# Optimization experiments

Hardware: AMD Instinct MI355X
Metric: run time of the kernel (lower is better)

Reference implementation:

```python
import jax, jax.numpy as jnp
import numpy as np

NP, P, H, NB = 14, 16, 12, 6  # n_patches per side, patch size, heads, blocks
HD, EMB, SEQ = 64, 768, NP * NP + 1


def _layernorm(x, g, b, eps=1e-5):
    m = x.mean(axis=-1, keepdims=True)
    v = x.var(axis=-1, keepdims=True)
    return (x - m) * jax.lax.rsqrt(v + eps) * g + b


def setup_inputs() -> dict:
    key = jax.random.key(0)
    ks = jax.random.split(key, 16)
    s = 0.02
    B = 64
    inp = {
        "images": jax.random.normal(ks[0], (B, 3, 224, 224), jnp.float32),
        "Wmap": jax.random.normal(ks[1], (768, 768), jnp.float32) * s,
        "bmap": jnp.zeros((768,), jnp.float32),
        "cls_tok": jax.random.normal(ks[2], (1, 768), jnp.float32) * s,
        "pos": jax.random.normal(ks[3], (SEQ, 768), jnp.float32) * s,
        "ln1_g": jnp.ones((NB, 768), jnp.float32),
        "ln1_b": jnp.zeros((NB, 768), jnp.float32),
        "Wq": jax.random.normal(ks[4], (NB, H, HD, HD), jnp.float32) * s,
        "bq": jnp.zeros((NB, H, HD), jnp.float32),
        "Wk": jax.random.normal(ks[5], (NB, H, HD, HD), jnp.float32) * s,
        "bk": jnp.zeros((NB, H, HD), jnp.float32),
        "Wv": jax.random.normal(ks[6], (NB, H, HD, HD), jnp.float32) * s,
        "bv": jnp.zeros((NB, H, HD), jnp.float32),
        "ln2_g": jnp.ones((NB, 768), jnp.float32),
        "ln2_b": jnp.zeros((NB, 768), jnp.float32),
        "W1": jax.random.normal(ks[7], (NB, 768, 3072), jnp.float32) * s,
        "b1": jnp.zeros((NB, 3072), jnp.float32),
        "W2": jax.random.normal(ks[8], (NB, 3072, 768), jnp.float32) * s,
        "b2": jnp.zeros((NB, 768), jnp.float32),
        "Whead": jax.random.normal(ks[9], (768, 10), jnp.float32) * s,
        "bhead": jnp.zeros((10,), jnp.float32),
    }
    return inp


def reference(images, Wmap, bmap, cls_tok, pos, ln1_g, ln1_b, Wq, bq, Wk, bk,
              Wv, bv, ln2_g, ln2_b, W1, b1, W2, b2, Whead, bhead):
    B = images.shape[0]
    # patchify: (B,3,224,224) -> (B,196,768); per-patch channel-first flatten
    x = images.reshape(B, 3, NP, P, NP, P)
    x = x.transpose(0, 2, 4, 1, 3, 5).reshape(B, NP * NP, 3 * P * P)
    tokens = x @ Wmap + bmap  # (B,196,768)
    tokens = jnp.concatenate(
        [jnp.broadcast_to(cls_tok[None], (B, 1, EMB)), tokens], axis=1)
    out = tokens + pos[None]  # (B,197,768)
    scale = 1.0 / jnp.sqrt(jnp.asarray(H, out.dtype))  # NOTE: source divides by sqrt(num_heads)
    for i in range(NB):
        h = _layernorm(out, ln1_g[i], ln1_b[i])
        xh = h.reshape(B, SEQ, H, HD)
        q = jnp.einsum('bshd,hde->bshe', xh, Wq[i]) + bq[i]
        k = jnp.einsum('bshd,hde->bshe', xh, Wk[i]) + bk[i]
        v = jnp.einsum('bshd,hde->bshe', xh, Wv[i]) + bv[i]
        attn = jax.nn.softmax(
            jnp.einsum('bqhd,bkhd->bhqk', q, k) * scale, axis=-1)
        o = jnp.einsum('bhqk,bkhd->bqhd', attn, v).reshape(B, SEQ, EMB)
        out = out + o
        h2 = _layernorm(out, ln2_g[i], ln2_b[i])
        mlp = jax.nn.gelu(h2 @ W1[i] + b1[i], approximate=False) @ W2[i] + b2[i]
        out = out + mlp
    cls = out[:, 0]  # (B,768)
    return jax.nn.softmax(cls @ Whead + bhead, axis=-1)
```

## Files before the change

### kernel.cpp

```cpp
#include <hip/hip_runtime.h>
#include <cstddef>

#define BATCH 64
#define SEQL  197
#define EMB   768
#define NH    12
#define HDIM  64
#define NBLK  6
#define MLPD  3072
#define TOKS  12608
#define PTOK  12544
#define ATT_SCALE 0.28867513459481287f
#define LOG2E 1.4426950408889634f

typedef short bf16x8 __attribute__((ext_vector_type(8)));
typedef float f32x4  __attribute__((ext_vector_type(4)));

__device__ inline float bf2f(unsigned short u) {
  union { unsigned int i; float f; } c; c.i = ((unsigned int)u) << 16; return c.f;
}
__device__ inline unsigned short f2bf(float f) {
  union { float f; unsigned int i; } c; c.f = f;
  unsigned int r = c.i + 0x7FFFu + ((c.i >> 16) & 1u);
  return (unsigned short)(r >> 16);
}

__device__ __forceinline__ float gelu_f(float x) {
  float u = __builtin_fabsf(x) * 0.70710678118654752f;
  float t = __builtin_amdgcn_rcpf(__builtin_fmaf(0.3275911f, u, 1.0f));
  float p = __builtin_fmaf(1.061405429f, t, -1.453152027f);
  p = __builtin_fmaf(p, t, 1.421413741f);
  p = __builtin_fmaf(p, t, -0.284496736f);
  p = __builtin_fmaf(p, t, 0.254829592f);
  p = p * t;
  float e = __expf(-u * u);
  float er = __builtin_fmaf(-p, e, 1.0f);
  er = __builtin_copysignf(er, x);
  return 0.5f * x * (1.0f + er);
}

__device__ __forceinline__ void gload16(const unsigned short* g, void* l) {
  __builtin_amdgcn_global_load_lds(
      (const __attribute__((address_space(1))) unsigned int*)g,
      (__attribute__((address_space(3))) unsigned int*)l, 16, 0, 0);
}

__global__ __launch_bounds__(256) void patchify_kernel(const float* __restrict__ img,
                                                       unsigned short* __restrict__ out) {
  int i4 = blockIdx.x * 256 + threadIdx.x;
  int f4 = i4 % 192;
  int r  = i4 / 192;
  int b  = r / 196, t = r - b * 196;
  int f  = f4 * 4;
  int c  = f >> 8;
  int rem = f & 255;
  int iy = rem >> 4, ix = rem & 15;
  int py = t / 14, px = t - py * 14;
  const float* src = img + ((((size_t)b * 3 + c) * 224 + py * 16 + iy) * 224 + px * 16 + ix);
  float4 v = *(const float4*)src;
  ushort4 u;
  u.x = f2bf(v.x); u.y = f2bf(v.y); u.z = f2bf(v.z); u.w = f2bf(v.w);
  *(ushort4*)(out + (size_t)r * 768 + f) = u;
}

__global__ __launch_bounds__(256) void clspos_kernel(const float* __restrict__ cls,
                                                     const float* __restrict__ pos,
                                                     float* __restrict__ X) {
  int idx = blockIdx.x * 256 + threadIdx.x;
  int b = idx / 768, e = idx - b * 768;
  X[(size_t)b * SEQL * 768 + e] = cls[e] + pos[e];
}

__global__ __launch_bounds__(256) void wconv_kernel(const float* __restrict__ W,
                                                    unsigned short* __restrict__ Wt,
                                                    int K, int N) {
  __shared__ float t[32][33];
  int k0 = blockIdx.x * 32, n0 = blockIdx.y * 32;
  int kk = threadIdx.x >> 3, nn = (threadIdx.x & 7) * 4;
  float4 v = *(const float4*)&W[(size_t)(k0 + kk) * N + n0 + nn];
  t[nn + 0][kk] = v.x; t[nn + 1][kk] = v.y; t[nn + 2][kk] = v.z; t[nn + 3][kk] = v.w;
  __syncthreads();
  int nr = threadIdx.x >> 3, kc = (threadIdx.x & 7) * 4;
  ushort4 u;
  u.x = f2bf(t[nr][kc + 0]); u.y = f2bf(t[nr][kc + 1]);
  u.z = f2bf(t[nr][kc + 2]); u.w = f2bf(t[nr][kc + 3]);
  *(ushort4*)&Wt[(size_t)(n0 + nr) * K + k0 + kc] = u;
}

__global__ __launch_bounds__(256) void qwconv_kernel(const float* __restrict__ Wq,
                                                     const float* __restrict__ Wk,
                                                     const float* __restrict__ Wv,
                                                     unsigned short* __restrict__ Wt) {
  int mh = blockIdx.x;
  int m = mh / 12, h = mh - m * 12;
  const float* src = (m == 0 ? Wq : (m == 1 ? Wk : Wv)) + (size_t)h * 4096;
  unsigned short* dst = Wt + (size_t)mh * 4096;
  for (int idx = threadIdx.x; idx < 4096; idx += 256) {
    int d = idx >> 6, e = idx & 63;
    dst[e * 64 + d] = f2bf(src[idx]);
  }
}

template<int MODE>
__global__ __launch_bounds__(256) void gemm_mfma(const unsigned short* __restrict__ A, int lda,
                                                 const unsigned short* __restrict__ Bt, int ldb,
                                                 void* __restrict__ Cv,
                                                 const float* __restrict__ bias,
                                                 const float* __restrict__ pos,
                                                 int M, int N, int K) {
  __shared__ short As[8192];
  __shared__ short Bs[8192];
  const int tid  = threadIdx.x;
  const int wid  = tid >> 6, lane = tid & 63;
  const int wr   = wid >> 1, wc = wid & 1;
  const int fr   = lane & 15;
  const int fq   = lane >> 4;
  const int m0   = blockIdx.y * 128;
  const int n0   = blockIdx.x * 128;
  const int srow = lane >> 3;
  const int schk = lane & 7;
  const int Mc   = M - 1;

  f32x4 acc[4][4];
#pragma unroll
  for (int m = 0; m < 4; ++m)
#pragma unroll
    for (int n = 0; n < 4; ++n) acc[m][n] = (f32x4)0.f;

  for (int k0 = 0; k0 < K; k0 += 64) {
#pragma unroll
    for (int i = 0; i < 4; ++i) {
      int row = i * 32 + wid * 8 + srow;
      int gr = m0 + row; if (gr > Mc) gr = Mc;
      gload16(A + (size_t)gr * lda + k0 + ((schk ^ (row & 7)) << 3),
              (char*)As + i * 4096 + wid * 1024);
      gload16(Bt + (size_t)(n0 + row) * ldb + k0 + ((schk ^ (row & 7)) << 3),
              (char*)Bs + i * 4096 + wid * 1024);
    }
    __syncthreads();
#pragma unroll
    for (int ks = 0; ks < 2; ++ks) {
      bf16x8 af[4], bfr[4];
#pragma unroll
      for (int m = 0; m < 4; ++m) {
        int row = (wr << 6) + (m << 4) + fr;
        int ch = ((ks << 2) + fq) ^ (row & 7);
        af[m] = *(const bf16x8*)&As[(row << 6) + (ch << 3)];
      }
#pragma unroll
      for (int n = 0; n < 4; ++n) {
        int row = (wc << 6) + (n << 4) + fr;
        int ch = ((ks << 2) + fq) ^ (row & 7);
        bfr[n] = *(const bf16x8*)&Bs[(row << 6) + (ch << 3)];
      }
#pragma unroll
      for (int m = 0; m < 4; ++m)
#pragma unroll
        for (int n = 0; n < 4; ++n)
          acc[m][n] = __builtin_amdgcn_mfma_f32_16x16x32_bf16(af[m], bfr[n], acc[m][n], 0, 0, 0);
    }
    __syncthreads();
  }

#pragma unroll
  for (int m = 0; m < 4; ++m) {
#pragma unroll
    for (int j = 0; j < 4; ++j) {
      int r = m0 + (wr << 6) + (m << 4) + (fq << 2) + j;
      if (r >= M) continue;
#pragma unroll
      for (int n = 0; n < 4; ++n) {
        int c = n0 + (wc << 6) + (n << 4) + fr;
        float v = acc[m][n][j] + bias[c];
        if (MODE == 0) {
          int b = r / 196, t = r - b * 196;
          ((float*)Cv)[((size_t)b * SEQL + 1 + t) * 768 + c] = v + pos[(size_t)(1 + t) * 768 + c];
        } else if (MODE == 1) {
          ((unsigned short*)Cv)[(size_t)r * MLPD + c] = f2bf(gelu_f(v));
        } else {
          ((float*)Cv)[(size_t)r * 768 + c] += v;
        }
      }
    }
  }
}

__global__ __launch_bounds__(256) void ln_kernel(const float* __restrict__ Xi,
                                                 unsigned short* __restrict__ Ho,
                                                 const float* __restrict__ g,
                                                 const float* __restrict__ bb) {
  int tok = blockIdx.x * 4 + (threadIdx.x >> 6);
  int lane = threadIdx.x & 63;
  const float* x = Xi + (size_t)tok * 768;
  float4 v0 = *(const float4*)(x + lane * 4);
  float4 v1 = *(const float4*)(x + 256 + lane * 4);
  float4 v2 = *(const float4*)(x + 512 + lane * 4);
  float s = v0.x + v0.y + v0.z + v0.w + v1.x + v1.y + v1.z + v1.w + v2.x + v2.y + v2.z + v2.w;
  float q = v0.x*v0.x + v0.y*v0.y + v0.z*v0.z + v0.w*v0.w
          + v1.x*v1.x + v1.y*v1.y + v1.z*v1.z + v1.w*v1.w
          + v2.x*v2.x + v2.y*v2.y + v2.z*v2.z + v2.w*v2.w;
#pragma unroll
  for (int o = 32; o > 0; o >>= 1) { s += __shfl_xor(s, o); q += __shfl_xor(q, o); }
  float mean = s * (1.f / 768.f);
  float var  = q * (1.f / 768.f) - mean * mean;
  float rs = rsqrtf(var + 1e-5f);
  unsigned short* outp = Ho + (size_t)tok * 768;
  float4 g0 = *(const float4*)(g + lane * 4);
  float4 g1 = *(const float4*)(g + 256 + lane * 4);
  float4 g2 = *(const float4*)(g + 512 + lane * 4);
  float4 b0 = *(const float4*)(bb + lane * 4);
  float4 b1 = *(const float4*)(bb + 256 + lane * 4);
  float4 b2 = *(const float4*)(bb + 512 + lane * 4);
  ushort4 s0, s1, s2;
  s0.x = f2bf((v0.x - mean) * rs * g0.x + b0.x); s0.y = f2bf((v0.y - mean) * rs * g0.y + b0.y);
  s0.z = f2bf((v0.z - mean) * rs * g0.z + b0.z); s0.w = f2bf((v0.w - mean) * rs * g0.w + b0.w);
  s1.x = f2bf((v1.x - mean) * rs * g1.x + b1.x); s1.y = f2bf((v1.y - mean) * rs * g1.y + b1.y);
  s1.z = f2bf((v1.z - mean) * rs * g1.z + b1.z); s1.w = f2bf((v1.w - mean) * rs * g1.w + b1.w);
  s2.x = f2bf((v2.x - mean) * rs * g2.x + b2.x); s2.y = f2bf((v2.y - mean) * rs * g2.y + b2.y);
  s2.z = f2bf((v2.z - mean) * rs * g2.z + b2.z); s2.w = f2bf((v2.w - mean) * rs * g2.w + b2.w);
  *(ushort4*)(outp + lane * 4) = s0;
  *(ushort4*)(outp + 256 + lane * 4) = s1;
  *(ushort4*)(outp + 512 + lane * 4) = s2;
}

__global__ __launch_bounds__(256) void qkv_mfma(const unsigned short* __restrict__ Hb,
    const unsigned short* __restrict__ Wt,
    const float* __restrict__ bq, const float* __restrict__ bk, const float* __restrict__ bv,
    unsigned short* __restrict__ Qo, unsigned short* __restrict__ Ko,
    unsigned short* __restrict__ Vo) {
  const int h = blockIdx.y;
  const int tid = threadIdx.x, wv = tid >> 6, lane = tid & 63;
  const int fr = lane & 15, hi = lane >> 4;
  const int t0 = blockIdx.x * 64 + wv * 16;
  const unsigned short* arow = Hb + (size_t)(t0 + fr) * 768 + h * 64;
  bf16x8 a0 = *(const bf16x8*)(arow + hi * 8);
  bf16x8 a1 = *(const bf16x8*)(arow + 32 + hi * 8);
  f32x4 acc[3][4];
#pragma unroll
  for (int m = 0; m < 3; ++m)
#pragma unroll
    for (int n = 0; n < 4; ++n) acc[m][n] = (f32x4)0.f;
#pragma unroll
  for (int m = 0; m < 3; ++m) {
    const unsigned short* wb = Wt + (size_t)(m * 12 + h) * 4096;
#pragma unroll
    for (int n = 0; n < 4; ++n) {
      bf16x8 b0 = *(const bf16x8*)&wb[(n * 16 + fr) * 64 + hi * 8];
      bf16x8 b1 = *(const bf16x8*)&wb[(n * 16 + fr) * 64 + 32 + hi * 8];
      acc[m][n] = __builtin_amdgcn_mfma_f32_16x16x32_bf16(a0, b0, acc[m][n], 0, 0, 0);
      acc[m][n] = __builtin_amdgcn_mfma_f32_16x16x32_bf16(a1, b1, acc[m][n], 0, 0, 0);
    }
  }
#pragma unroll
  for (int m = 0; m < 3; ++m) {
    const float* bptr = (m == 0 ? bq : (m == 1 ? bk : bv)) + h * 64;
    unsigned short* optr = (m == 0 ? Qo : (m == 1 ? Ko : Vo));
    const float sc = (m == 0) ? ATT_SCALE : 1.f;
#pragma unroll
    for (int j = 0; j < 4; ++j) {
      int tk = t0 + hi * 4 + j;
      int b = tk / 197, s = tk - b * 197;
      size_t base_o = (((size_t)b * NH + h) * SEQL + s) * 64;
#pragma unroll
      for (int n = 0; n < 4; ++n)
        optr[base_o + n * 16 + fr] = f2bf((acc[m][n][j] + bptr[n * 16 + fr]) * sc);
    }
  }
}

__global__ __launch_bounds__(256) void attn_kernel(const unsigned short* __restrict__ Q,
                                                   const unsigned short* __restrict__ Kg,
                                                   const unsigned short* __restrict__ Vg,
                                                   float* __restrict__ X) {
  __shared__ unsigned short Vt[64][232];
  __shared__ unsigned short Pl[4][16][232];
  const int bh = blockIdx.x;
  const int b = bh / NH, h = bh - b * NH;
  const int tid = threadIdx.x, wv = tid >> 6, lane = tid & 63;
  const int fr = lane & 15, hi = lane >> 4;
  const unsigned short* Qp = Q  + (size_t)bh * SEQL * 64;
  const unsigned short* Kp = Kg + (size_t)bh * SEQL * 64;
  const unsigned short* Vp = Vg + (size_t)bh * SEQL * 64;

  for (int idx = tid; idx < SEQL * 16; idx += 256) {
    int s = idx >> 4, d4 = (idx & 15) * 4;
    ushort4 v = *(const ushort4*)&Vp[s * 64 + d4];
    Vt[d4 + 0][s] = v.x; Vt[d4 + 1][s] = v.y; Vt[d4 + 2][s] = v.z; Vt[d4 + 3][s] = v.w;
  }
  for (int idx = tid; idx < 64 * 35; idx += 256) {
    int d = idx / 35, c = 197 + idx % 35;
    Vt[d][c] = 0;
  }
  for (int idx = lane; idx < 16 * 24; idx += 64) {
    int r = idx / 24, c = 208 + idx % 24;
    Pl[wv][r][c] = 0;
  }
  __syncthreads();

  for (int qt = wv; qt < 13; qt += 4) {
    int qrow = qt * 16 + fr; if (qrow > 196) qrow = 196;
    bf16x8 qa0 = *(const bf16x8*)&Qp[qrow * 64 + hi * 8];
    bf16x8 qa1 = *(const bf16x8*)&Qp[qrow * 64 + 32 + hi * 8];
    f32x4 sc[13];
#pragma unroll
    for (int kt = 0; kt < 13; ++kt) {
      int krow = kt * 16 + fr; if (krow > 196) krow = 196;
      bf16x8 kb0 = *(const bf16x8*)&Kp[krow * 64 + hi * 8];
      bf16x8 kb1 = *(const bf16x8*)&Kp[krow * 64 + 32 + hi * 8];
      f32x4 a = (f32x4)0.f;
      a = __builtin_amdgcn_mfma_f32_16x16x32_bf16(qa0, kb0, a, 0, 0, 0);
      a = __builtin_amdgcn_mfma_f32_16x16x32_bf16(qa1, kb1, a, 0, 0, 0);
      sc[kt] = a;
    }
    float mx[4] = {-3e38f, -3e38f, -3e38f, -3e38f};
#pragma unroll
    for (int kt = 0; kt < 13; ++kt) {
      bool inval = (kt == 12) && (fr >= 5);
#pragma unroll
      for (int j = 0; j < 4; ++j) {
        float s = inval ? -3e38f : sc[kt][j];
        sc[kt][j] = s;
        mx[j] = fmaxf(mx[j], s);
      }
    }
#pragma unroll
    for (int o = 8; o > 0; o >>= 1)
#pragma unroll
      for (int j = 0; j < 4; ++j) mx[j] = fmaxf(mx[j], __shfl_xor(mx[j], o));
    float l[4] = {0.f, 0.f, 0.f, 0.f};
#pragma unroll
    for (int kt = 0; kt < 13; ++kt) {
#pragma unroll
      for (int j = 0; j < 4; ++j) {
        float p = exp2f((sc[kt][j] - mx[j]) * LOG2E);
        if ((kt == 12) && (fr >= 5)) p = 0.f;
        l[j] += p;
        Pl[wv][hi * 4 + j][kt * 16 + fr] = f2bf(p);
      }
    }
#pragma unroll
    for (int o = 8; o > 0; o >>= 1)
#pragma unroll
      for (int j = 0; j < 4; ++j) l[j] += __shfl_xor(l[j], o);
    f32x4 ov[4];
#pragma unroll
    for (int n = 0; n < 4; ++n) ov[n] = (f32x4)0.f;
#pragma unroll
    for (int kc = 0; kc < 7; ++kc) {
      bf16x8 pa = *(const bf16x8*)&Pl[wv][fr][kc * 32 + hi * 8];
#pragma unroll
      for (int n = 0; n < 4; ++n) {
        bf16x8 vb = *(const bf16x8*)&Vt[n * 16 + fr][kc * 32 + hi * 8];
        ov[n] = __builtin_amdgcn_mfma_f32_16x16x32_bf16(pa, vb, ov[n], 0, 0, 0);
      }
    }
#pragma unroll
    for (int j = 0; j < 4; ++j) {
      int r = qt * 16 + hi * 4 + j;
      if (r >= SEQL) continue;
      float inv = 1.f / l[j];
      float* xp = X + ((size_t)b * SEQL + r) * 768 + h * 64 + fr;
#pragma unroll
      for (int n = 0; n < 4; ++n) xp[n * 16] += ov[n][j] * inv;
    }
  }
}

__global__ __launch_bounds__(64) void head_kernel(const float* __restrict__ X,
                                                  const float* __restrict__ Wh,
                                                  const float* __restrict__ bh,
                                                  float* __restrict__ out) {
  __shared__ float lg[10];
  int b = blockIdx.x, t = threadIdx.x;
  if (t < 10) {
    float acc = bh[t];
    const float* x = X + (size_t)b * SEQL * 768;
    for (int d = 0; d < 768; ++d) acc += x[d] * Wh[d * 10 + t];
    lg[t] = acc;
  }
  __syncthreads();
  if (t == 0) {
    float m = lg[0];
    for (int c = 1; c < 10; ++c) m = fmaxf(m, lg[c]);
    float ssum = 0.f;
    for (int c = 0; c < 10; ++c) ssum += expf(lg[c] - m);
    for (int c = 0; c < 10; ++c) out[b * 10 + c] = expf(lg[c] - m) / ssum;
  }
}

extern "C" void kernel_launch(void* const* d_in, const int* in_sizes, int n_in,
                              void* d_out, int out_size, void* d_ws, size_t ws_size,
                              hipStream_t stream) {
  const float* images = (const float*)d_in[0];
  const float* Wmap = (const float*)d_in[1];
  const float* bmap = (const float*)d_in[2];
  const float* cls  = (const float*)d_in[3];
  const float* pos  = (const float*)d_in[4];
  const float* ln1g = (const float*)d_in[5];
  const float* ln1b = (const float*)d_in[6];
  const float* Wq   = (const float*)d_in[7];
  const float* bq   = (const float*)d_in[8];
  const float* Wk   = (const float*)d_in[9];
  const float* bk   = (const float*)d_in[10];
  const float* Wv   = (const float*)d_in[11];
  const float* bv   = (const float*)d_in[12];
  const float* ln2g = (const float*)d_in[13];
  const float* ln2b = (const float*)d_in[14];
  const float* W1   = (const float*)d_in[15];
  const float* b1   = (const float*)d_in[16];
  const float* W2   = (const float*)d_in[17];
  const float* b2   = (const float*)d_in[18];
  const float* Wh   = (const float*)d_in[19];
  const float* bhd  = (const float*)d_in[20];
  float* out = (float*)d_out;

  const size_t ACT = (size_t)TOKS * 768;
  const size_t oX = 0;
  const size_t oHb = oX + ACT * 4;
  const size_t oR  = oHb + ACT * 2;
  const size_t oW1 = oR + 3 * ACT * 4;
  const size_t oW2 = oW1 + (size_t)768 * 3072 * 2;
  const size_t oWm = oW2 + (size_t)768 * 3072 * 2;
  const size_t oQW = oWm + (size_t)768 * 768 * 2;
  const size_t need = oQW + (size_t)36 * 4096 * 2;
  if (ws_size < need) return;

  char* ws = (char*)d_ws;
  float* X = (float*)(ws + oX);
  unsigned short* Hb = (unsigned short*)(ws + oHb);
  unsigned short* Qb = (unsigned short*)(ws + oR);
  unsigned short* Kb = Qb + ACT;
  unsigned short* Vb = Kb + ACT;
  unsigned short* mid = (unsigned short*)(ws + oR);
  unsigned short* patches = (unsigned short*)(ws + oR);
  unsigned short* W1t = (unsigned short*)(ws + oW1);
  unsigned short* W2t = (unsigned short*)(ws + oW2);
  unsigned short* Wmapt = (unsigned short*)(ws + oWm);
  unsigned short* QWt = (unsigned short*)(ws + oQW);

  wconv_kernel<<<dim3(24, 24), 256, 0, stream>>>(Wmap, Wmapt, 768, 768);
  patchify_kernel<<<9408, 256, 0, stream>>>(images, patches);
  clspos_kernel<<<192, 256, 0, stream>>>(cls, pos, X);
  gemm_mfma<0><<<dim3(6, 98), 256, 0, stream>>>(patches, 768, Wmapt, 768, X, bmap, pos,
                                                PTOK, 768, 768);

  for (int i = 0; i < NBLK; ++i) {
    ln_kernel<<<3152, 256, 0, stream>>>(X, Hb, ln1g + i * 768, ln1b + i * 768);
    qwconv_kernel<<<36, 256, 0, stream>>>(Wq + (size_t)i * 49152, Wk + (size_t)i * 49152,
                                          Wv + (size_t)i * 49152, QWt);
    qkv_mfma<<<dim3(197, 12), 256, 0, stream>>>(Hb, QWt,
        bq + i * 768, bk + i * 768, bv + i * 768, Qb, Kb, Vb);
    attn_kernel<<<768, 256, 0, stream>>>(Qb, Kb, Vb, X);
    ln_kernel<<<3152, 256, 0, stream>>>(X, Hb, ln2g + i * 768, ln2b + i * 768);
    wconv_kernel<<<dim3(24, 96), 256, 0, stream>>>(W1 + (size_t)i * 2359296, W1t, 768, MLPD);
    wconv_kernel<<<dim3(96, 24), 256, 0, stream>>>(W2 + (size_t)i * 2359296, W2t, MLPD, 768);
    gemm_mfma<1><<<dim3(24, 99), 256, 0, stream>>>(Hb, 768, W1t, 768, mid, b1 + i * MLPD,
                                                   nullptr, TOKS, MLPD, 768);
    gemm_mfma<2><<<dim3(6, 99), 256, 0, stream>>>(mid, MLPD, W2t, MLPD, X, b2 + i * 768,
                                                  nullptr, TOKS, 768, MLPD);
  }
  head_kernel<<<64, 64, 0, stream>>>(X, Wh, bhd, out);
}
```

Measured before the change: 1.920 ms.

## Vectorize GELU and Q/K epilogue stores via column-permuted layouts

The MLP1 epilogue now packs four bf16 outputs per lane into one ushort4 store. This places columns in a permuted order within each 64-column group of the intermediate activation, and W2 is converted with a matching K-permutation so the second GEMM still computes the right contraction. Q and K are stored the same way with a permuted head dimension, which cancels in the QK dot product, while V keeps the original layout. The aim is fewer, wider global stores, in exchange for a layout coupling across kernels that must stay consistent.

```diff
diff --git a/kernel.cpp b/kernel.cpp
--- a/kernel.cpp
+++ b/kernel.cpp
@@ -73,7 +73,7 @@
 
 __global__ __launch_bounds__(256) void wconv_kernel(const float* __restrict__ W,
                                                     unsigned short* __restrict__ Wt,
-                                                    int K, int N) {
+                                                    int K, int N, int perm) {
   __shared__ float t[32][33];
   int k0 = blockIdx.x * 32, n0 = blockIdx.y * 32;
   int kk = threadIdx.x >> 3, nn = (threadIdx.x & 7) * 4;
@@ -84,7 +84,17 @@
   ushort4 u;
   u.x = f2bf(t[nr][kc + 0]); u.y = f2bf(t[nr][kc + 1]);
   u.z = f2bf(t[nr][kc + 2]); u.w = f2bf(t[nr][kc + 3]);
-  *(ushort4*)&Wt[(size_t)(n0 + nr) * K + k0 + kc] = u;
+  if (!perm) {
+    *(ushort4*)&Wt[(size_t)(n0 + nr) * K + k0 + kc] = u;
+  } else {
+    size_t base = (size_t)(n0 + nr) * K + (size_t)(k0 & ~63);
+    int klo = (k0 & 32) + kc;
+    size_t st = base + (size_t)((klo & 15) * 4 + (klo >> 4));
+    Wt[st + 0]  = u.x;
+    Wt[st + 4]  = u.y;
+    Wt[st + 8]  = u.z;
+    Wt[st + 12] = u.w;
+  }
 }
 
 __global__ __launch_bounds__(256) void qwconv_kernel(const float* __restrict__ Wq,
@@ -168,17 +178,28 @@
     for (int j = 0; j < 4; ++j) {
       int r = m0 + (wr << 6) + (m << 4) + (fq << 2) + j;
       if (r >= M) continue;
-#pragma unroll
-      for (int n = 0; n < 4; ++n) {
-        int c = n0 + (wc << 6) + (n << 4) + fr;
-        float v = acc[m][n][j] + bias[c];
-        if (MODE == 0) {
-          int b = r / 196, t = r - b * 196;
-          ((float*)Cv)[((size_t)b * SEQL + 1 + t) * 768 + c] = v + pos[(size_t)(1 + t) * 768 + c];
-        } else if (MODE == 1) {
-          ((unsigned short*)Cv)[(size_t)r * MLPD + c] = f2bf(gelu_f(v));
-        } else {
-          ((float*)Cv)[(size_t)r * 768 + c] += v;
+      if (MODE == 1) {
+        ushort4 q;
+        float v0 = acc[0 * 0 + m][0][j] + bias[n0 + (wc << 6) + 0 * 16 + fr];
+        float v1 = acc[m][1][j] + bias[n0 + (wc << 6) + 1 * 16 + fr];
+        float v2 = acc[m][2][j] + bias[n0 + (wc << 6) + 2 * 16 + fr];
+        float v3 = acc[m][3][j] + bias[n0 + (wc << 6) + 3 * 16 + fr];
+        q.x = f2bf(gelu_f(v0));
+        q.y = f2bf(gelu_f(v1));
+        q.z = f2bf(gelu_f(v2));
+        q.w = f2bf(gelu_f(v3));
+        *(ushort4*)&((unsigned short*)Cv)[(size_t)r * MLPD + n0 + (wc << 6) + fr * 4] = q;
+      } else {
+#pragma unroll
+        for (int n = 0; n < 4; ++n) {
+          int c = n0 + (wc << 6) + (n << 4) + fr;
+          float v = acc[m][n][j] + bias[c];
+          if (MODE == 0) {
+            int b = r / 196, t = r - b * 196;
+            ((float*)Cv)[((size_t)b * SEQL + 1 + t) * 768 + c] = v + pos[(size_t)(1 + t) * 768 + c];
+          } else {
+            ((float*)Cv)[(size_t)r * 768 + c] += v;
+          }
         }
       }
     }
@@ -261,9 +282,18 @@
       int tk = t0 + hi * 4 + j;
       int b = tk / 197, s = tk - b * 197;
       size_t base_o = (((size_t)b * NH + h) * SEQL + s) * 64;
-#pragma unroll
-      for (int n = 0; n < 4; ++n)
-        optr[base_o + n * 16 + fr] = f2bf((acc[m][n][j] + bptr[n * 16 + fr]) * sc);
+      if (m < 2) {
+        ushort4 o;
+        o.x = f2bf((acc[m][0][j] + bptr[0 * 16 + fr]) * sc);
+        o.y = f2bf((acc[m][1][j] + bptr[1 * 16 + fr]) * sc);
+        o.z = f2bf((acc[m][2][j] + bptr[2 * 16 + fr]) * sc);
+        o.w = f2bf((acc[m][3][j] + bptr[3 * 16 + fr]) * sc);
+        *(ushort4*)&optr[base_o + fr * 4] = o;
+      } else {
+#pragma unroll
+        for (int n = 0; n < 4; ++n)
+          optr[base_o + n * 16 + fr] = f2bf(acc[m][n][j] + bptr[n * 16 + fr]);
+      }
     }
   }
 }
@@ -438,7 +468,7 @@
   unsigned short* Wmapt = (unsigned short*)(ws + oWm);
   unsigned short* QWt = (unsigned short*)(ws + oQW);
 
-  wconv_kernel<<<dim3(24, 24), 256, 0, stream>>>(Wmap, Wmapt, 768, 768);
+  wconv_kernel<<<dim3(24, 24), 256, 0, stream>>>(Wmap, Wmapt, 768, 768, 0);
   patchify_kernel<<<9408, 256, 0, stream>>>(images, patches);
   clspos_kernel<<<192, 256, 0, stream>>>(cls, pos, X);
   gemm_mfma<0><<<dim3(6, 98), 256, 0, stream>>>(patches, 768, Wmapt, 768, X, bmap, pos,
@@ -452,8 +482,8 @@
         bq + i * 768, bk + i * 768, bv + i * 768, Qb, Kb, Vb);
     attn_kernel<<<768, 256, 0, stream>>>(Qb, Kb, Vb, X);
     ln_kernel<<<3152, 256, 0, stream>>>(X, Hb, ln2g + i * 768, ln2b + i * 768);
-    wconv_kernel<<<dim3(24, 96), 256, 0, stream>>>(W1 + (size_t)i * 2359296, W1t, 768, MLPD);
-    wconv_kernel<<<dim3(96, 24), 256, 0, stream>>>(W2 + (size_t)i * 2359296, W2t, MLPD, 768);
+    wconv_kernel<<<dim3(24, 96), 256, 0, stream>>>(W1 + (size_t)i * 2359296, W1t, 768, MLPD, 0);
+    wconv_kernel<<<dim3(96, 24), 256, 0, stream>>>(W2 + (size_t)i * 2359296, W2t, MLPD, 768, 1);
     gemm_mfma<1><<<dim3(24, 99), 256, 0, stream>>>(Hb, 768, W1t, 768, mid, b1 + i * MLPD,
                                                    nullptr, TOKS, MLPD, 768);
     gemm_mfma<2><<<dim3(6, 99), 256, 0, stream>>>(mid, MLPD, W2t, MLPD, X, b2 + i * 768,
```

After: 1.914 ms. No clear change (-0.3%).
